# Performance work log

Hardware: AMD Instinct MI355X
Metric: run time of the kernel (lower is better)

The kernel has to match this reference:

```python
import jax, jax.numpy as jnp
import numpy as np

MAX_DEG = 3
DEG_DIMS = [1, 3, 5, 7]          # degree_to_dim(d) = 2d+1
SUM_DIM = 16                     # sum of DEG_DIMS
FREQ_SUM = 44                    # sum over (d_in,d_out) of 2*min(d_in,d_out)+1
C = 32                           # channels per degree (in == out, FULL fusion)
EDGE_DIM = 2                     # fiber_edge[0] + 1
MID = 32                         # RadialProfile mid_dim
E = 4096
N = 1024


def setup_inputs() -> dict:
    key = jax.random.key(0)
    ks = jax.random.split(key, 16)
    inp = {}
    for d, dim in enumerate(DEG_DIMS):
        inp[f"node_feats_{d}"] = jax.random.normal(ks[d], (N, C, dim), jnp.float32)
    inp["edge_feats_0"] = jax.random.normal(ks[4], (E, EDGE_DIM, 1), jnp.float32)
    inp["basis"] = jax.random.normal(ks[5], (E, SUM_DIM, FREQ_SUM, SUM_DIM), jnp.float32)
    inp["src"] = jax.random.randint(ks[6], (E,), 0, N, dtype=jnp.int32)
    inp["dst"] = jax.random.randint(ks[7], (E,), 0, N, dtype=jnp.int32)
    # RadialProfile params: Linear(2,32) -> ReLU -> Linear(32,32) -> ReLU -> Linear(32, 44*32*32, bias=False)
    inp["w1"] = jax.random.normal(ks[8], (EDGE_DIM, MID), jnp.float32) / np.sqrt(EDGE_DIM)
    inp["b1"] = jnp.zeros((MID,), jnp.float32)
    inp["w2"] = jax.random.normal(ks[9], (MID, MID), jnp.float32) / np.sqrt(MID)
    inp["b2"] = jnp.zeros((MID,), jnp.float32)
    inp["w3"] = jax.random.normal(ks[10], (MID, FREQ_SUM * C * C), jnp.float32) / np.sqrt(MID)
    # self-interaction kernels per output degree
    for d in range(MAX_DEG + 1):
        inp[f"kernel_self_{d}"] = jax.random.normal(ks[11 + d], (C, C), jnp.float32) / np.sqrt(C)
    return inp


def _conv_se3(node_feats, edge_feats_0, basis, src, dst,
              w1, b1, w2, b2, w3, kernels_self):
    e = edge_feats_0.shape[0]
    # invariant edge feats: [E, edge_dim]
    inv = edge_feats_0[..., 0]
    # gather source node features and fuse along representation dim: [E, C, 16]
    feats = jnp.concatenate([nf[src] for nf in node_feats], axis=-1)
    # RadialProfile MLP -> radial weights [E, C_out, C_in * FREQ_SUM]
    h = jax.nn.relu(inv @ w1 + b1)
    h = jax.nn.relu(h @ w2 + b2)
    radial_weights = (h @ w3).reshape(e, C, C * FREQ_SUM)
    # VersatileConvSE3 fused path:
    # tmp = (features @ basis_view).view(E, C*FREQ_SUM, SUM_DIM)
    basis_view = basis.reshape(e, SUM_DIM, FREQ_SUM * SUM_DIM)
    tmp = jnp.einsum('eci,eix->ecx', feats, basis_view).reshape(e, C * FREQ_SUM, SUM_DIM)
    out_fused = jnp.einsum('eok,eks->eos', radial_weights, tmp)  # [E, C, 16]
    # unfuse by degree, add self-interaction at dst, pool (copy_e_sum) to nodes
    outs = []
    off = 0
    for d, dim in enumerate(DEG_DIMS):
        o = out_fused[..., off:off + dim]
        o = o + jnp.einsum('oc,ecd->eod', kernels_self[d], node_feats[d][dst])
        outs.append(jax.ops.segment_sum(o, dst, num_segments=N))
        off += dim
    # return fused node output [N, C, 16] (concat of degrees 0..3)
    return jnp.concatenate(outs, axis=-1)


def reference(node_feats_0, node_feats_1, node_feats_2, node_feats_3,
              edge_feats_0, basis, src, dst,
              w1, b1, w2, b2, w3,
              kernel_self_0, kernel_self_1, kernel_self_2, kernel_self_3):
    return _conv_se3([node_feats_0, node_feats_1, node_feats_2, node_feats_3],
                     edge_feats_0, basis, src, dst,
                     w1, b1, w2, b2, w3,
                     [kernel_self_0, kernel_self_1, kernel_self_2, kernel_self_3])
```

## Files before the change

kernel.cpp:

```cpp
#include <hip/hip_runtime.h>
#include <hip/hip_bf16.h>

#define NN 1024
#define EE 4096
#define CC 32
#define SD 16
#define FQ 44
#define MIDC 32
#define EB 16
#define NFQ 2
#define FPB 22

typedef short s16x4 __attribute__((ext_vector_type(4)));
typedef short s16x8 __attribute__((ext_vector_type(8)));
typedef float fx4 __attribute__((ext_vector_type(4)));

__device__ __forceinline__ unsigned short f2b(float x) {
    __hip_bfloat16 b = __float2bfloat16(x);
    return *reinterpret_cast<unsigned short*>(&b);
}

__global__ __launch_bounds__(256) void k_w3t2(const float* __restrict__ w3,
                                              unsigned short* __restrict__ w3t2) {
    int tid = blockIdx.x * 256 + threadIdx.x;
    int m = tid & 31;
    int o = (tid >> 5) & 31;
    int c = tid >> 10;
    const float* rp = &w3[(size_t)m * 45056 + o * 1408 + c * 44];
    float v[44];
#pragma unroll
    for (int q = 0; q < 11; q++) {
        float4 t4 = *(const float4*)(rp + q * 4);
        v[q * 4 + 0] = t4.x; v[q * 4 + 1] = t4.y;
        v[q * 4 + 2] = t4.z; v[q * 4 + 3] = t4.w;
    }
#pragma unroll
    for (int f = 0; f < FQ; f++) {
        w3t2[(((size_t)f * CC + o) * CC + c) * CC + m] = f2b(v[f]);
    }
}

__global__ __launch_bounds__(256) void k_h(const float* __restrict__ ef,
                                           const float* __restrict__ w1,
                                           const float* __restrict__ b1,
                                           const float* __restrict__ w2,
                                           const float* __restrict__ b2,
                                           const int* __restrict__ dst,
                                           unsigned short* __restrict__ h2,
                                           int* __restrict__ deg) {
    int e = blockIdx.x * 256 + threadIdx.x;
    if (e >= EE) return;
    float i0 = ef[e * 2 + 0], i1 = ef[e * 2 + 1];
    float h1[MIDC];
#pragma unroll
    for (int j = 0; j < MIDC; j++) {
        float v = i0 * w1[j] + i1 * w1[MIDC + j] + b1[j];
        h1[j] = v > 0.f ? v : 0.f;
    }
    for (int j = 0; j < MIDC; j++) {
        float v = b2[j];
#pragma unroll
        for (int m = 0; m < MIDC; m++) v += h1[m] * w2[m * MIDC + j];
        v = v > 0.f ? v : 0.f;
        h2[e * MIDC + j] = f2b(v);
    }
    atomicAdd(&deg[dst[e]], 1);
}

__global__ __launch_bounds__(512, 4) void k_main(
    const float* __restrict__ nf0, const float* __restrict__ nf1,
    const float* __restrict__ nf2, const float* __restrict__ nf3,
    const float* __restrict__ basis, const int* __restrict__ src,
    const int* __restrict__ dst, const unsigned short* __restrict__ h2,
    const unsigned short* __restrict__ w3t2, float* __restrict__ out) {
    __shared__ __align__(16) unsigned short rad_lds[EB * CC * CC];
    __shared__ __align__(16) unsigned short u_scr[16 * 640];

    int t = threadIdx.x;
    int wv = t >> 6;
    int l = t & 63;
    int l15 = l & 15;
    int kg = l >> 4;
    int eg = blockIdx.x >> 1;
    int fq = blockIdx.x & 1;
    int eb = eg * EB;
    int f0 = fq * FPB;

    float* fstage = (float*)rad_lds;
    {
        int e = t >> 5, c = t & 31;
        int sn = src[eb + e];
        float* row = &fstage[(e * CC + c) * SD];
        row[0] = nf0[sn * CC + c];
#pragma unroll
        for (int j = 0; j < 3; j++) row[1 + j] = nf1[(sn * CC + c) * 3 + j];
#pragma unroll
        for (int j = 0; j < 5; j++) row[4 + j] = nf2[(sn * CC + c) * 5 + j];
#pragma unroll
        for (int j = 0; j < 7; j++) row[9 + j] = nf3[(sn * CC + c) * 7 + j];
    }
    s16x8 h2frag = *(const s16x8*)(h2 + ((size_t)(eb + l15) * MIDC + (kg << 3)));
    __syncthreads();

    s16x8 feats[2][2];
#pragma unroll
    for (int ei = 0; ei < 2; ei++) {
        int e = (wv << 1) + ei;
#pragma unroll
        for (int ch = 0; ch < 2; ch++) {
            s16x8 fr = {};
            if (kg < 2) {
                const float4* fp4 =
                    (const float4*)&fstage[(e * CC + (ch << 4) + l15) * SD + (kg << 3)];
                float4 a = fp4[0], b = fp4[1];
                fr[0] = (short)f2b(a.x); fr[1] = (short)f2b(a.y);
                fr[2] = (short)f2b(a.z); fr[3] = (short)f2b(a.w);
                fr[4] = (short)f2b(b.x); fr[5] = (short)f2b(b.y);
                fr[6] = (short)f2b(b.z); fr[7] = (short)f2b(b.w);
            }
            feats[ei][ch] = fr;
        }
    }
    __syncthreads();

    fx4 acc[2][2];
#pragma unroll
    for (int q = 0; q < 4; q++) acc[q >> 1][q & 1] = (fx4){0.f, 0.f, 0.f, 0.f};
    fx4 zz = (fx4){0.f, 0.f, 0.f, 0.f};

    float pf[2][8];
#define ISSUE_PF(FNEXT)                                                                   \
    if (kg < 2) {                                                                         \
        _Pragma("unroll") for (int ei = 0; ei < 2; ei++) {                                \
            int e_ = (wv << 1) + ei;                                                      \
            const float* bp =                                                             \
                &basis[(((size_t)(eb + e_) * SD + (kg << 3)) * FQ + (FNEXT)) * SD + l15]; \
            _Pragma("unroll") for (int j = 0; j < 8; j++)                                 \
                pf[ei][j] = bp[(size_t)j * (FQ * SD)];                                    \
        }                                                                                 \
    }

    ISSUE_PF(f0);

    s16x8 bb[2];

    for (int fi = 0; fi < FPB; fi++) {
        int f = f0 + fi;

#pragma unroll
        for (int j = 0; j < 8; j++) {
            int o = (wv << 2) + (j >> 1);
            int ch = j & 1;
            s16x8 af = *(const s16x8*)(w3t2 +
                ((((size_t)f * CC + o) * CC + (ch << 4) + l15) * CC + (kg << 3)));
            fx4 cf = __builtin_amdgcn_mfma_f32_16x16x32_bf16(af, h2frag, zz, 0, 0, 0);
            int byte = (l15 << 11) + (o << 6) + (ch << 5) + (kg << 3);
            byte ^= ((l15 ^ o) & 7) << 4;
            s16x4 pk;
            pk[0] = (short)f2b(cf[0]); pk[1] = (short)f2b(cf[1]);
            pk[2] = (short)f2b(cf[2]); pk[3] = (short)f2b(cf[3]);
            *(s16x4*)((char*)rad_lds + byte) = pk;
        }

#pragma unroll
        for (int ei = 0; ei < 2; ei++) {
            s16x8 b = {};
            if (kg < 2) {
#pragma unroll
                for (int j = 0; j < 8; j++) b[j] = (short)f2b(pf[ei][j]);
            }
            bb[ei] = b;
        }
        __syncthreads();

        if (fi + 1 < FPB) { ISSUE_PF(f + 1); }

        fx4 u[2][2];
#pragma unroll
        for (int ei = 0; ei < 2; ei++) {
#pragma unroll
            for (int ch = 0; ch < 2; ch++)
                u[ei][ch] = __builtin_amdgcn_mfma_f32_16x16x32_bf16(feats[ei][ch], bb[ei], zz, 0, 0, 0);
        }
#pragma unroll
        for (int ei = 0; ei < 2; ei++) {
            int rbase = ((wv << 1) + ei) * 1280;
#pragma unroll
            for (int ch = 0; ch < 2; ch++) {
                s16x4 pk;
                pk[0] = (short)f2b(u[ei][ch][0]); pk[1] = (short)f2b(u[ei][ch][1]);
                pk[2] = (short)f2b(u[ei][ch][2]); pk[3] = (short)f2b(u[ei][ch][3]);
                *(s16x4*)((char*)u_scr + rbase + l15 * 80 + (ch << 5) + (kg << 3)) = pk;
            }
        }
#pragma unroll
        for (int ei = 0; ei < 2; ei++) {
            int e = (wv << 1) + ei;
            int rbase = ((wv << 1) + ei) * 1280;
            s16x8 ub = *(const s16x8*)((char*)u_scr + rbase + l15 * 80 + (kg << 4));
#pragma unroll
            for (int oh = 0; oh < 2; oh++) {
                int o = (oh << 4) + l15;
                int abyte = (e << 11) + (o << 6) + (kg << 4);
                abyte ^= ((e ^ o) & 7) << 4;
                s16x8 ra = *(const s16x8*)((char*)rad_lds + abyte);
                acc[ei][oh] =
                    __builtin_amdgcn_mfma_f32_16x16x32_bf16(ra, ub, acc[ei][oh], 0, 0, 0);
            }
        }
        __syncthreads();
    }

#pragma unroll
    for (int ei = 0; ei < 2; ei++) {
        int e = (wv << 1) + ei;
        int d = dst[eb + e];
        float* op = &out[(size_t)d * (CC * SD)];
#pragma unroll
        for (int oh = 0; oh < 2; oh++) {
#pragma unroll
            for (int r = 0; r < 4; r++) {
                int o = (oh << 4) + (kg << 2) + r;
                atomicAdd(&op[o * SD + l15], acc[ei][oh][r]);
            }
        }
    }
}

__global__ __launch_bounds__(256) void k_self(
    const float* __restrict__ nf0, const float* __restrict__ nf1,
    const float* __restrict__ nf2, const float* __restrict__ nf3,
    const float* __restrict__ ks0, const float* __restrict__ ks1,
    const float* __restrict__ ks2, const float* __restrict__ ks3,
    const int* __restrict__ deg, float* __restrict__ out) {
    int idx = blockIdx.x * 256 + threadIdx.x;
    if (idx >= NN * CC * SD) return;
    int n = idx >> 9;
    int rem = idx & 511;
    int o = rem >> 4;
    int s = rem & 15;
    const float* nf;
    const float* ks;
    int dim, off;
    if (s < 1) { nf = nf0; ks = ks0; dim = 1; off = 0; }
    else if (s < 4) { nf = nf1; ks = ks1; dim = 3; off = 1; }
    else if (s < 9) { nf = nf2; ks = ks2; dim = 5; off = 4; }
    else { nf = nf3; ks = ks3; dim = 7; off = 9; }
    int j = s - off;
    float acc = 0.f;
#pragma unroll
    for (int c = 0; c < CC; c++) acc += ks[o * CC + c] * nf[(n * CC + c) * dim + j];
    out[idx] += (float)deg[n] * acc;
}

extern "C" void kernel_launch(void* const* d_in, const int* in_sizes, int n_in,
                              void* d_out, int out_size, void* d_ws, size_t ws_size,
                              hipStream_t stream) {
    const float* nf0 = (const float*)d_in[0];
    const float* nf1 = (const float*)d_in[1];
    const float* nf2 = (const float*)d_in[2];
    const float* nf3 = (const float*)d_in[3];
    const float* ef = (const float*)d_in[4];
    const float* basis = (const float*)d_in[5];
    const int* src = (const int*)d_in[6];
    const int* dst = (const int*)d_in[7];
    const float* w1 = (const float*)d_in[8];
    const float* b1 = (const float*)d_in[9];
    const float* w2 = (const float*)d_in[10];
    const float* b2 = (const float*)d_in[11];
    const float* w3 = (const float*)d_in[12];
    const float* ks0 = (const float*)d_in[13];
    const float* ks1 = (const float*)d_in[14];
    const float* ks2 = (const float*)d_in[15];
    const float* ks3 = (const float*)d_in[16];
    float* out = (float*)d_out;

    unsigned short* h2 = (unsigned short*)d_ws;
    int* deg = (int*)((char*)d_ws + EE * MIDC * 2);
    unsigned short* w3t2 = (unsigned short*)((char*)d_ws + EE * MIDC * 2 + 4096);

    hipMemsetAsync(d_out, 0, (size_t)out_size * sizeof(float), stream);
    hipMemsetAsync(deg, 0, NN * sizeof(int), stream);

    k_w3t2<<<128, 256, 0, stream>>>(w3, w3t2);
    k_h<<<EE / 256, 256, 0, stream>>>(ef, w1, b1, w2, b2, dst, h2, deg);
    k_main<<<(EE / EB) * NFQ, 512, 0, stream>>>(nf0, nf1, nf2, nf3, basis, src, dst,
                                                h2, w3t2, out);
    k_self<<<(NN * CC * SD) / 256, 256, 0, stream>>>(nf0, nf1, nf2, nf3, ks0, ks1,
                                                     ks2, ks3, deg, out);
}
```

Baseline: 137.5 us.

## Use 16x16x16 MFMA to drop u scratch LDS round-trip and prefetch w3 fragments

Replaces the feature×basis 16x16x32 MFMA, which half-wasted its K dimension, with 16x16x16 MFMAs whose output layout feeds the radial MFMA directly. This removes the u_scr LDS write/read and the feature staging through LDS, and drops two __syncthreads. Node features are now gathered straight from global memory into registers. It also software-prefetches the next frequency's w3t2 fragments along with the basis values, changes the LDS swizzle to a 16-way XOR, and precomputes the LDS addresses. In exchange it issues more, smaller MFMAs and holds more registers for the prefetched fragments, which may hurt occupancy.

```diff
diff --git a/kernel.cpp b/kernel.cpp
--- a/kernel.cpp
+++ b/kernel.cpp
@@ -18,6 +18,25 @@
 __device__ __forceinline__ unsigned short f2b(float x) {
     __hip_bfloat16 b = __float2bfloat16(x);
     return *reinterpret_cast<unsigned short*>(&b);
+}
+
+__device__ __forceinline__ s16x4 pack4(float a, float b, float c, float d) {
+    s16x4 r;
+    r[0] = (short)f2b(a); r[1] = (short)f2b(b);
+    r[2] = (short)f2b(c); r[3] = (short)f2b(d);
+    return r;
+}
+
+__device__ __forceinline__ fx4 mfma16(s16x4 a, s16x4 b, fx4 c) {
+#if defined(__HIP_DEVICE_COMPILE__)
+#if __has_builtin(__builtin_amdgcn_mfma_f32_16x16x16_bf16)
+    return __builtin_amdgcn_mfma_f32_16x16x16_bf16(a, b, c, 0, 0, 0);
+#else
+    return __builtin_amdgcn_mfma_f32_16x16x16bf16_1k(a, b, c, 0, 0, 0);
+#endif
+#else
+    return c;
+#endif
 }
 
 __global__ __launch_bounds__(256) void k_w3t2(const float* __restrict__ w3,
@@ -74,7 +93,6 @@
     const int* __restrict__ dst, const unsigned short* __restrict__ h2,
     const unsigned short* __restrict__ w3t2, float* __restrict__ out) {
     __shared__ __align__(16) unsigned short rad_lds[EB * CC * CC];
-    __shared__ __align__(16) unsigned short u_scr[16 * 640];
 
     int t = threadIdx.x;
     int wv = t >> 6;
@@ -86,126 +104,108 @@
     int eb = eg * EB;
     int f0 = fq * FPB;
 
-    float* fstage = (float*)rad_lds;
-    {
-        int e = t >> 5, c = t & 31;
-        int sn = src[eb + e];
-        float* row = &fstage[(e * CC + c) * SD];
-        row[0] = nf0[sn * CC + c];
-#pragma unroll
-        for (int j = 0; j < 3; j++) row[1 + j] = nf1[(sn * CC + c) * 3 + j];
-#pragma unroll
-        for (int j = 0; j < 5; j++) row[4 + j] = nf2[(sn * CC + c) * 5 + j];
-#pragma unroll
-        for (int j = 0; j < 7; j++) row[9 + j] = nf3[(sn * CC + c) * 7 + j];
-    }
     s16x8 h2frag = *(const s16x8*)(h2 + ((size_t)(eb + l15) * MIDC + (kg << 3)));
-    __syncthreads();
-
-    s16x8 feats[2][2];
+
+    s16x4 fa[2][2];
+#pragma unroll
+    for (int ei = 0; ei < 2; ei++) {
+        int sn = src[eb + (wv << 1) + ei];
+#pragma unroll
+        for (int ch = 0; ch < 2; ch++) {
+            int c = (ch << 4) + l15;
+            s16x4 v;
+#pragma unroll
+            for (int j = 0; j < 4; j++) {
+                int i = (kg << 2) + j;
+                float x;
+                if (i < 1) x = nf0[sn * CC + c];
+                else if (i < 4) x = nf1[(sn * CC + c) * 3 + (i - 1)];
+                else if (i < 9) x = nf2[(sn * CC + c) * 5 + (i - 4)];
+                else x = nf3[(sn * CC + c) * 7 + (i - 9)];
+                v[j] = (short)f2b(x);
+            }
+            fa[ei][ch] = v;
+        }
+    }
+
+    int radw[8];
+#pragma unroll
+    for (int j = 0; j < 8; j++) {
+        int o = (wv << 2) + (j >> 1), ch = j & 1;
+        int b = (l15 << 11) | (o << 6) | (ch << 5) | (kg << 3);
+        radw[j] = b ^ (((l15 ^ o) & 15) << 3);
+    }
+    int rada[2][2][2];
 #pragma unroll
     for (int ei = 0; ei < 2; ei++) {
         int e = (wv << 1) + ei;
 #pragma unroll
-        for (int ch = 0; ch < 2; ch++) {
-            s16x8 fr = {};
-            if (kg < 2) {
-                const float4* fp4 =
-                    (const float4*)&fstage[(e * CC + (ch << 4) + l15) * SD + (kg << 3)];
-                float4 a = fp4[0], b = fp4[1];
-                fr[0] = (short)f2b(a.x); fr[1] = (short)f2b(a.y);
-                fr[2] = (short)f2b(a.z); fr[3] = (short)f2b(a.w);
-                fr[4] = (short)f2b(b.x); fr[5] = (short)f2b(b.y);
-                fr[6] = (short)f2b(b.z); fr[7] = (short)f2b(b.w);
-            }
-            feats[ei][ch] = fr;
-        }
-    }
-    __syncthreads();
+        for (int oh = 0; oh < 2; oh++) {
+            int o = (oh << 4) + l15;
+#pragma unroll
+            for (int ch = 0; ch < 2; ch++) {
+                int b = (e << 11) | (o << 6) | (ch << 5) | (kg << 3);
+                rada[ei][oh][ch] = b ^ (((e ^ o) & 15) << 3);
+            }
+        }
+    }
 
     fx4 acc[2][2];
 #pragma unroll
     for (int q = 0; q < 4; q++) acc[q >> 1][q & 1] = (fx4){0.f, 0.f, 0.f, 0.f};
     fx4 zz = (fx4){0.f, 0.f, 0.f, 0.f};
 
-    float pf[2][8];
-#define ISSUE_PF(FNEXT)                                                                   \
-    if (kg < 2) {                                                                         \
-        _Pragma("unroll") for (int ei = 0; ei < 2; ei++) {                                \
-            int e_ = (wv << 1) + ei;                                                      \
-            const float* bp =                                                             \
-                &basis[(((size_t)(eb + e_) * SD + (kg << 3)) * FQ + (FNEXT)) * SD + l15]; \
-            _Pragma("unroll") for (int j = 0; j < 8; j++)                                 \
-                pf[ei][j] = bp[(size_t)j * (FQ * SD)];                                    \
-        }                                                                                 \
-    }
-
-    ISSUE_PF(f0);
-
-    s16x8 bb[2];
+    s16x8 w[8];
+    float pf[2][4];
+
+#define LOAD_W(F)                                                                       \
+    {                                                                                   \
+        _Pragma("unroll") for (int j = 0; j < 8; j++) {                                 \
+            int o_ = (wv << 2) + (j >> 1), ch_ = j & 1;                                 \
+            w[j] = *(const s16x8*)(w3t2 +                                               \
+                ((((size_t)(F) * CC + o_) * CC + (ch_ << 4) + l15) * CC + (kg << 3)));  \
+        }                                                                               \
+    }
+#define LOAD_PF(F)                                                                      \
+    {                                                                                   \
+        _Pragma("unroll") for (int ei_ = 0; ei_ < 2; ei_++) {                           \
+            const float* bp = basis +                                                   \
+                (((size_t)(eb + (wv << 1) + ei_) * SD + (kg << 2)) * FQ + (F)) * SD +   \
+                l15;                                                                    \
+            _Pragma("unroll") for (int j = 0; j < 4; j++)                               \
+                pf[ei_][j] = bp[(size_t)j * (FQ * SD)];                                 \
+        }                                                                               \
+    }
+
+    LOAD_W(f0);
+    LOAD_PF(f0);
 
     for (int fi = 0; fi < FPB; fi++) {
-        int f = f0 + fi;
-
 #pragma unroll
         for (int j = 0; j < 8; j++) {
-            int o = (wv << 2) + (j >> 1);
-            int ch = j & 1;
-            s16x8 af = *(const s16x8*)(w3t2 +
-                ((((size_t)f * CC + o) * CC + (ch << 4) + l15) * CC + (kg << 3)));
-            fx4 cf = __builtin_amdgcn_mfma_f32_16x16x32_bf16(af, h2frag, zz, 0, 0, 0);
-            int byte = (l15 << 11) + (o << 6) + (ch << 5) + (kg << 3);
-            byte ^= ((l15 ^ o) & 7) << 4;
-            s16x4 pk;
-            pk[0] = (short)f2b(cf[0]); pk[1] = (short)f2b(cf[1]);
-            pk[2] = (short)f2b(cf[2]); pk[3] = (short)f2b(cf[3]);
-            *(s16x4*)((char*)rad_lds + byte) = pk;
-        }
+            fx4 cf = __builtin_amdgcn_mfma_f32_16x16x32_bf16(w[j], h2frag, zz, 0, 0, 0);
+            *(s16x4*)((char*)rad_lds + radw[j]) = pack4(cf[0], cf[1], cf[2], cf[3]);
+        }
+        s16x4 bbf[2];
+#pragma unroll
+        for (int ei = 0; ei < 2; ei++)
+            bbf[ei] = pack4(pf[ei][0], pf[ei][1], pf[ei][2], pf[ei][3]);
+        int fn = (fi + 1 < FPB) ? f0 + fi + 1 : f0;
+        LOAD_W(fn);
+        LOAD_PF(fn);
+        __syncthreads();
 
 #pragma unroll
         for (int ei = 0; ei < 2; ei++) {
-            s16x8 b = {};
-            if (kg < 2) {
-#pragma unroll
-                for (int j = 0; j < 8; j++) b[j] = (short)f2b(pf[ei][j]);
-            }
-            bb[ei] = b;
-        }
-        __syncthreads();
-
-        if (fi + 1 < FPB) { ISSUE_PF(f + 1); }
-
-        fx4 u[2][2];
-#pragma unroll
-        for (int ei = 0; ei < 2; ei++) {
-#pragma unroll
-            for (int ch = 0; ch < 2; ch++)
-                u[ei][ch] = __builtin_amdgcn_mfma_f32_16x16x32_bf16(feats[ei][ch], bb[ei], zz, 0, 0, 0);
-        }
-#pragma unroll
-        for (int ei = 0; ei < 2; ei++) {
-            int rbase = ((wv << 1) + ei) * 1280;
 #pragma unroll
             for (int ch = 0; ch < 2; ch++) {
-                s16x4 pk;
-                pk[0] = (short)f2b(u[ei][ch][0]); pk[1] = (short)f2b(u[ei][ch][1]);
-                pk[2] = (short)f2b(u[ei][ch][2]); pk[3] = (short)f2b(u[ei][ch][3]);
-                *(s16x4*)((char*)u_scr + rbase + l15 * 80 + (ch << 5) + (kg << 3)) = pk;
-            }
-        }
-#pragma unroll
-        for (int ei = 0; ei < 2; ei++) {
-            int e = (wv << 1) + ei;
-            int rbase = ((wv << 1) + ei) * 1280;
-            s16x8 ub = *(const s16x8*)((char*)u_scr + rbase + l15 * 80 + (kg << 4));
-#pragma unroll
-            for (int oh = 0; oh < 2; oh++) {
-                int o = (oh << 4) + l15;
-                int abyte = (e << 11) + (o << 6) + (kg << 4);
-                abyte ^= ((e ^ o) & 7) << 4;
-                s16x8 ra = *(const s16x8*)((char*)rad_lds + abyte);
-                acc[ei][oh] =
-                    __builtin_amdgcn_mfma_f32_16x16x32_bf16(ra, ub, acc[ei][oh], 0, 0, 0);
+                fx4 u = mfma16(fa[ei][ch], bbf[ei], zz);
+                s16x4 ub = pack4(u[0], u[1], u[2], u[3]);
+#pragma unroll
+                for (int oh = 0; oh < 2; oh++) {
+                    s16x4 ra = *(const s16x4*)((char*)rad_lds + rada[ei][oh][ch]);
+                    acc[ei][oh] = mfma16(ra, ub, acc[ei][oh]);
+                }
             }
         }
         __syncthreads();
@@ -279,8 +279,8 @@
     int* deg = (int*)((char*)d_ws + EE * MIDC * 2);
     unsigned short* w3t2 = (unsigned short*)((char*)d_ws + EE * MIDC * 2 + 4096);
 
-    hipMemsetAsync(d_out, 0, (size_t)out_size * sizeof(float), stream);
-    hipMemsetAsync(deg, 0, NN * sizeof(int), stream);
+    (void)hipMemsetAsync(d_out, 0, (size_t)out_size * sizeof(float), stream);
+    (void)hipMemsetAsync(deg, 0, NN * sizeof(int), stream);
 
     k_w3t2<<<128, 256, 0, stream>>>(w3, w3t2);
     k_h<<<EE / 256, 256, 0, stream>>>(ef, w1, b1, w2, b2, dst, h2, deg);
```

Result: faster. 112.6 us (-18.1%).
